# Optimization experiments

Measured on AMD Instinct MI355X. Metric: run time of the kernel, lower is better.

The kernel has to match this reference:

```python
import jax, jax.numpy as jnp
import numpy as np

HEAD_SIZE = 64


def setup_inputs() -> dict:
    key = jax.random.key(0)
    ks = jax.random.split(key, 4)
    B, S, H, D = 8, 4096, 768, HEAD_SIZE
    scale = 1.0 / np.sqrt(H)
    return {
        "x": jax.random.normal(ks[0], (B, S, H), dtype=jnp.float32),
        "Wq": jax.random.normal(ks[1], (H, D), dtype=jnp.float32) * scale,
        "bq": jnp.zeros((D,), dtype=jnp.float32),
        "Wk": jax.random.normal(ks[2], (H, D), dtype=jnp.float32) * scale,
        "bk": jnp.zeros((D,), dtype=jnp.float32),
        "Wv": jax.random.normal(ks[3], (H, D), dtype=jnp.float32) * scale,
        "bv": jnp.zeros((D,), dtype=jnp.float32),
    }


def reference(x, Wq, bq, Wk, bk, Wv, bv):
    # x: [B, S, H]
    B, S, H = x.shape
    D = Wq.shape[1]
    q = x @ Wq + bq  # [B, S, D]
    k = x @ Wk + bk
    v = x @ Wv + bv
    # naive full score matrix [B, S, S]
    scores = jnp.einsum("bsd,btd->bst", q, k)
    causal = jnp.tril(jnp.ones((S, S), dtype=bool))  # lower-triangular mask
    scores = jnp.where(causal[None, :, :], scores, -jnp.inf)
    attn = jax.nn.softmax(scores / jnp.sqrt(jnp.float32(D)), axis=-1)
    # dropout is identity in eval/deterministic reference
    out = jnp.einsum("bst,btd->bsd", attn, v)  # [B, S, D]
    return out
```

## Files before the change

kernel.cpp:

```cpp
#include <hip/hip_runtime.h>

typedef unsigned short u16;
typedef __bf16 bf16_t;
typedef bf16_t bf16x8 __attribute__((ext_vector_type(8)));
typedef float f32x4 __attribute__((ext_vector_type(4)));
typedef u16 u16x8 __attribute__((ext_vector_type(8)));

#define B_ 8
#define S_ 4096
#define H_ 768
#define M_ (B_ * S_)

__device__ __forceinline__ u16 f2b(float f) {
  unsigned u = __float_as_uint(f);
  u += 0x7fffu + ((u >> 16) & 1u);
  return (u16)(u >> 16);
}

__device__ __forceinline__ void gl_lds16(const void* g, void* l) {
  __builtin_amdgcn_global_load_lds(
      (const __attribute__((address_space(1))) void*)g,
      (__attribute__((address_space(3))) void*)l, 16, 0, 0);
}

__global__ __launch_bounds__(256) void wconv_k(const float* __restrict__ Wq,
                                               const float* __restrict__ Wk,
                                               const float* __restrict__ Wv,
                                               u16* __restrict__ WbT) {
  __shared__ float wt[64 * 68];
  const int tid = threadIdx.x;
  int mat = blockIdx.x / 12;
  int k0 = (blockIdx.x % 12) * 64;
  const float* W = (mat == 0) ? Wq : ((mat == 1) ? Wk : Wv);
  int r = tid >> 2, c0 = (tid & 3) * 16;
  const float* src = W + (size_t)(k0 + r) * 64 + c0;
#pragma unroll
  for (int j = 0; j < 16; j += 4)
    *(float4*)&wt[r * 68 + c0 + j] = *(const float4*)(src + j);
  __syncthreads();
  int d = tid >> 2;
  u16* dst = WbT + (size_t)(mat * 64 + d) * 768 + k0 + c0;
  u16x8 o0, o1;
#pragma unroll
  for (int j = 0; j < 8; ++j) o0[j] = f2b(wt[(c0 + j) * 68 + d]);
#pragma unroll
  for (int j = 0; j < 8; ++j) o1[j] = f2b(wt[(c0 + 8 + j) * 68 + d]);
  *(u16x8*)dst = o0;
  *(u16x8*)(dst + 8) = o1;
}

__global__ __launch_bounds__(256) void qkv_k(const float* __restrict__ x,
                                             const u16* __restrict__ WbT,
                                             const float* __restrict__ bq,
                                             const float* __restrict__ bk,
                                             const float* __restrict__ bv,
                                             u16* __restrict__ qb,
                                             u16* __restrict__ kb,
                                             u16* __restrict__ vbT) {
  __shared__ __align__(16) u16 smem[2 * 2560 + 2 * 7680];
  const int tid = threadIdx.x;
  const int w = tid >> 6, ln = tid & 15, qd = (tid >> 4) & 3;
  const int row0 = blockIdx.x * 64;

  const f32x4 z4 = {0.f, 0.f, 0.f, 0.f};
  f32x4 acc[4][3];
#pragma unroll
  for (int rt = 0; rt < 4; ++rt)
#pragma unroll
    for (int ct = 0; ct < 3; ++ct) acc[rt][ct] = z4;

  const int xr = tid >> 2, xc = (tid & 3) * 8;
  float4 xf0, xf1;
  u16x8 wf[3];

  auto load_t = [&](int kt) {
    const float* sx = x + (size_t)(row0 + xr) * 768 + kt * 32 + xc;
    xf0 = *(const float4*)sx;
    xf1 = *(const float4*)(sx + 4);
#pragma unroll
    for (int i = 0; i < 3; ++i) {
      int c = i * 256 + tid;
      int r = c >> 2, off = (c & 3) * 8;
      wf[i] = *(const u16x8*)(WbT + (size_t)r * 768 + kt * 32 + off);
    }
  };

  load_t(0);
  for (int kt = 0; kt < 24; ++kt) {
    u16* xs = smem + (kt & 1) * 2560;
    u16* wsb = smem + 5120 + (kt & 1) * 7680;
    {
      u16x8 v;
      v[0] = f2b(xf0.x); v[1] = f2b(xf0.y); v[2] = f2b(xf0.z); v[3] = f2b(xf0.w);
      v[4] = f2b(xf1.x); v[5] = f2b(xf1.y); v[6] = f2b(xf1.z); v[7] = f2b(xf1.w);
      *(u16x8*)&xs[xr * 40 + xc] = v;
#pragma unroll
      for (int i = 0; i < 3; ++i) {
        int c = i * 256 + tid;
        int r = c >> 2, off = (c & 3) * 8;
        *(u16x8*)&wsb[r * 40 + off] = wf[i];
      }
    }
    if (kt < 23) load_t(kt + 1);
    __syncthreads();
    bf16x8 af[4], bfr[3];
#pragma unroll
    for (int rt = 0; rt < 4; ++rt)
      af[rt] = *(const bf16x8*)&xs[(rt * 16 + ln) * 40 + qd * 8];
#pragma unroll
    for (int ct = 0; ct < 3; ++ct)
      bfr[ct] = *(const bf16x8*)&wsb[(w * 48 + ct * 16 + ln) * 40 + qd * 8];
#pragma unroll
    for (int rt = 0; rt < 4; ++rt)
#pragma unroll
      for (int ct = 0; ct < 3; ++ct)
        acc[rt][ct] = __builtin_amdgcn_mfma_f32_16x16x32_bf16(
            af[rt], bfr[ct], acc[rt][ct], 0, 0, 0);
    __syncthreads();
  }

  u16* vt = smem;
#pragma unroll
  for (int ct = 0; ct < 3; ++ct) {
    int col = w * 48 + ct * 16 + ln;
    int mat = col >> 6, d = col & 63;
    if (mat < 2) {
      const float* bp = (mat == 0) ? bq : bk;
      u16* op = (mat == 0) ? qb : kb;
      float bias = bp[d];
      float scale = (mat == 0) ? 0.18033688011112042f : 1.0f;
#pragma unroll
      for (int rt = 0; rt < 4; ++rt)
#pragma unroll
        for (int r = 0; r < 4; ++r)
          op[(size_t)(row0 + rt * 16 + qd * 4 + r) * 64 + d] =
              f2b((acc[rt][ct][r] + bias) * scale);
    } else {
      float bias = bv[d];
#pragma unroll
      for (int rt = 0; rt < 4; ++rt)
#pragma unroll
        for (int r = 0; r < 4; ++r)
          vt[d * 72 + rt * 16 + qd * 4 + r] = f2b(acc[rt][ct][r] + bias);
    }
  }
  __syncthreads();
  {
    int d = tid >> 2, so = (tid & 3) * 16;
    int b = row0 >> 12, s0 = row0 & 4095;
    u16* dst = vbT + ((size_t)b * 64 + d) * 4096 + s0 + so;
    *(u16x8*)dst = *(const u16x8*)&vt[d * 72 + so];
    *(u16x8*)(dst + 8) = *(const u16x8*)&vt[d * 72 + so + 8];
  }
}

__global__ __launch_bounds__(256) void attn_k(const u16* __restrict__ qb,
                                              const u16* __restrict__ kb,
                                              const u16* __restrict__ vbT,
                                              float* __restrict__ po0,
                                              float* __restrict__ po1,
                                              float* __restrict__ pl0,
                                              float* __restrict__ pl1) {
  __shared__ __align__(16) u16 ks[2][4096];
  __shared__ __align__(16) u16 vs[2][4096];
  __shared__ __align__(16) u16 ps[4 * 32 * 72];
  const int tid = threadIdx.x;
  const int w = tid >> 6, ln = tid & 15, qd = (tid >> 4) & 3;
  const int id = blockIdx.x;
  const int b = id & 7;
  const int j = id >> 3;
  const int qi = 31 - (j >> 1);
  const int chunk = j & 1;
  const int tstart = chunk ? (qi + 1) : 0;
  const int tcount = qi + 1;
  const int q0 = qi * 128;
  const int q0w = q0 + w * 32;
  const int base = b * S_;
  const u16* kg = kb + (size_t)base * 64;
  const u16* vg = vbT + (size_t)b * 64 * 4096;

  bf16x8 qf[2][2];
#pragma unroll
  for (int rt = 0; rt < 2; ++rt) {
    const u16* qrow = qb + (size_t)(base + q0w + rt * 16 + ln) * 64;
    qf[rt][0] = *(const bf16x8*)(qrow + qd * 8);
    qf[rt][1] = *(const bf16x8*)(qrow + 32 + qd * 8);
  }
  const f32x4 z4 = {0.f, 0.f, 0.f, 0.f};
  f32x4 o[2][4];
#pragma unroll
  for (int rt = 0; rt < 2; ++rt)
#pragma unroll
    for (int nt = 0; nt < 4; ++nt) o[rt][nt] = z4;
  float lp[2][4] = {{0.f, 0.f, 0.f, 0.f}, {0.f, 0.f, 0.f, 0.f}};
  u16* psw = ps + w * (32 * 72);
  const int lr = (tid & 63) >> 3, csl = tid & 7;

  auto prefetch = [&](int bufi, int tile) {
    const u16* kt_ = kg + (size_t)tile * 4096;
    const u16* vt_ = vg + tile * 64;
#pragma unroll
    for (int i = 0; i < 2; ++i) {
      int r0 = w * 16 + i * 8;
      int r = r0 + lr;
      int c = csl ^ (r & 7);
      gl_lds16(kt_ + r * 64 + c * 8, &ks[bufi][r0 * 64]);
      gl_lds16(vt_ + (size_t)r * 4096 + c * 8, &vs[bufi][r0 * 64]);
    }
  };

  prefetch(0, tstart);
  int buf = 0;
  for (int it = 0; it < tcount; ++it) {
    __syncthreads();
    if (it + 1 < tcount) prefetch(buf ^ 1, tstart + it + 1);
    const int t0a = (tstart + it) * 64;

    if (t0a <= q0w + 31) {
      f32x4 s0[4] = {z4, z4, z4, z4};
      f32x4 s1[4] = {z4, z4, z4, z4};
#pragma unroll
      for (int kc = 0; kc < 2; ++kc) {
        int cs = (kc * 4 + qd) ^ (ln & 7);
#pragma unroll
        for (int nt = 0; nt < 4; ++nt) {
          bf16x8 bfr = *(const bf16x8*)&ks[buf][(nt * 16 + ln) * 64 + cs * 8];
          s0[nt] = __builtin_amdgcn_mfma_f32_16x16x32_bf16(qf[0][kc], bfr, s0[nt], 0, 0, 0);
          s1[nt] = __builtin_amdgcn_mfma_f32_16x16x32_bf16(qf[1][kc], bfr, s1[nt], 0, 0, 0);
        }
      }
      if (t0a + 63 > q0w) {
#pragma unroll
        for (int nt = 0; nt < 4; ++nt) {
          int tg = t0a + nt * 16 + ln;
#pragma unroll
          for (int r = 0; r < 4; ++r) {
            if (tg > q0w + qd * 4 + r) s0[nt][r] = -INFINITY;
            if (tg > q0w + 16 + qd * 4 + r) s1[nt][r] = -INFINITY;
          }
        }
      }
#pragma unroll
      for (int nt = 0; nt < 4; ++nt)
#pragma unroll
        for (int r = 0; r < 4; ++r) {
          float p0 = __builtin_amdgcn_exp2f(s0[nt][r]);
          float p1 = __builtin_amdgcn_exp2f(s1[nt][r]);
          lp[0][r] += p0;
          lp[1][r] += p1;
          psw[(qd * 4 + r) * 72 + nt * 16 + ln] = f2b(p0);
          psw[(16 + qd * 4 + r) * 72 + nt * 16 + ln] = f2b(p1);
        }
#pragma unroll
      for (int kc = 0; kc < 2; ++kc) {
        bf16x8 a0 = *(const bf16x8*)&psw[ln * 72 + kc * 32 + qd * 8];
        bf16x8 a1 = *(const bf16x8*)&psw[(16 + ln) * 72 + kc * 32 + qd * 8];
        int cs = (kc * 4 + qd) ^ (ln & 7);
#pragma unroll
        for (int nt = 0; nt < 4; ++nt) {
          bf16x8 vfr = *(const bf16x8*)&vs[buf][(nt * 16 + ln) * 64 + cs * 8];
          o[0][nt] = __builtin_amdgcn_mfma_f32_16x16x32_bf16(a0, vfr, o[0][nt], 0, 0, 0);
          o[1][nt] = __builtin_amdgcn_mfma_f32_16x16x32_bf16(a1, vfr, o[1][nt], 0, 0, 0);
        }
      }
    }
    buf ^= 1;
  }

#pragma unroll
  for (int rt = 0; rt < 2; ++rt)
#pragma unroll
    for (int r = 0; r < 4; ++r) {
      float v = lp[rt][r];
      v += __shfl_xor(v, 1); v += __shfl_xor(v, 2);
      v += __shfl_xor(v, 4); v += __shfl_xor(v, 8);
      lp[rt][r] = v;
    }
  float* op = (tstart == 0) ? po0 : po1;
  float* lpt = (tstart == 0) ? pl0 : pl1;
#pragma unroll
  for (int rt = 0; rt < 2; ++rt)
#pragma unroll
    for (int r = 0; r < 4; ++r) {
      int row = base + q0w + rt * 16 + qd * 4 + r;
#pragma unroll
      for (int nt = 0; nt < 4; ++nt)
        op[(size_t)row * 64 + nt * 16 + ln] = o[rt][nt][r];
      if (ln == 0) lpt[row] = lp[rt][r];
    }
}

__global__ __launch_bounds__(256) void comb_k(const float* __restrict__ po0,
                                              const float* __restrict__ po1,
                                              const float* __restrict__ pl0,
                                              const float* __restrict__ pl1,
                                              float* __restrict__ out) {
  int idx = blockIdx.x * 256 + threadIdx.x;
  int r = idx >> 4, d0 = (idx & 15) * 4;
  float4 a = *(const float4*)(po0 + (size_t)r * 64 + d0);
  float4 c = *(const float4*)(po1 + (size_t)r * 64 + d0);
  float l = pl0[r] + pl1[r];
  float inv = 1.0f / l;
  a.x = (a.x + c.x) * inv;
  a.y = (a.y + c.y) * inv;
  a.z = (a.z + c.z) * inv;
  a.w = (a.w + c.w) * inv;
  *(float4*)(out + (size_t)r * 64 + d0) = a;
}

extern "C" void kernel_launch(void* const* d_in, const int* in_sizes, int n_in,
                              void* d_out, int out_size, void* d_ws, size_t ws_size,
                              hipStream_t stream) {
  const float* x  = (const float*)d_in[0];
  const float* Wq = (const float*)d_in[1];
  const float* bq = (const float*)d_in[2];
  const float* Wk = (const float*)d_in[3];
  const float* bk = (const float*)d_in[4];
  const float* Wv = (const float*)d_in[5];
  const float* bv = (const float*)d_in[6];
  float* out = (float*)d_out;

  char* wsp = (char*)d_ws;
  u16* WbT = (u16*)wsp;
  u16* qb  = (u16*)(wsp + 294912);
  u16* kb  = (u16*)(wsp + 4489216);
  u16* vbT = (u16*)(wsp + 8683520);
  float* po0 = (float*)(wsp + 12877824);
  float* po1 = (float*)(wsp + 21266432);
  float* pl0 = (float*)(wsp + 29655040);
  float* pl1 = (float*)(wsp + 29786112);

  hipLaunchKernelGGL(wconv_k, dim3(36), dim3(256), 0, stream, Wq, Wk, Wv, WbT);
  hipLaunchKernelGGL(qkv_k, dim3(512), dim3(256), 0, stream,
                     x, WbT, bq, bk, bv, qb, kb, vbT);
  hipLaunchKernelGGL(attn_k, dim3(512), dim3(256), 0, stream,
                     qb, kb, vbT, po0, po1, pl0, pl1);
  hipLaunchKernelGGL(comb_k, dim3(2048), dim3(256), 0, stream,
                     po0, po1, pl0, pl1, out);
}
```

Measured before the change: 234.1 us.

## Split attention KV range into variable chunks, triple-buffer tiles, transpose score MFMA

Replaces the fixed two-way split of each query block's key range with a variable number of chunks (1-4, scaled by causal length), launching 640 workgroups to balance work and fill the GPU better. The combine kernel sums the matching number of partial outputs and denominators. The K/V staging moves from double to triple buffering, with an explicit vmcnt wait instead of a full syncthreads. The QK MFMA operands are swapped so each lane holds a row's scores, which allows vectorized, XOR-swizzled P writes to LDS and fewer shuffles. The cost is more partial-output memory traffic and extra LDS use.

```diff
diff --git a/kernel.cpp b/kernel.cpp
--- a/kernel.cpp
+++ b/kernel.cpp
@@ -5,6 +5,7 @@
 typedef bf16_t bf16x8 __attribute__((ext_vector_type(8)));
 typedef float f32x4 __attribute__((ext_vector_type(4)));
 typedef u16 u16x8 __attribute__((ext_vector_type(8)));
+typedef u16 u16x4 __attribute__((ext_vector_type(4)));
 
 #define B_ 8
 #define S_ 4096
@@ -157,43 +158,46 @@
 __global__ __launch_bounds__(256) void attn_k(const u16* __restrict__ qb,
                                               const u16* __restrict__ kb,
                                               const u16* __restrict__ vbT,
-                                              float* __restrict__ po0,
-                                              float* __restrict__ po1,
-                                              float* __restrict__ pl0,
-                                              float* __restrict__ pl1) {
-  __shared__ __align__(16) u16 ks[2][4096];
-  __shared__ __align__(16) u16 vs[2][4096];
-  __shared__ __align__(16) u16 ps[4 * 32 * 72];
+                                              float* __restrict__ po,
+                                              float* __restrict__ pl) {
+  __shared__ __align__(16) u16 ks[3][4096];
+  __shared__ __align__(16) u16 vs[3][4096];
+  __shared__ __align__(16) u16 ps[4 * 32 * 64];
   const int tid = threadIdx.x;
-  const int w = tid >> 6, ln = tid & 15, qd = (tid >> 4) & 3;
+  const int wv = tid >> 6, ln = tid & 15, qd = (tid >> 4) & 3;
   const int id = blockIdx.x;
   const int b = id & 7;
   const int j = id >> 3;
-  const int qi = 31 - (j >> 1);
-  const int chunk = j & 1;
-  const int tstart = chunk ? (qi + 1) : 0;
-  const int tcount = qi + 1;
+  int qi = 31, acc = 0;
+  while (acc + ((qi >> 3) + 1) <= j) {
+    acc += (qi >> 3) + 1;
+    --qi;
+  }
+  const int c = j - acc;
+  const int ntiles = 2 * qi + 2;
+  const int nc = (qi >> 3) + 1;
+  const int bas = ntiles / nc, rem = ntiles % nc;
+  const int tstart = c * bas + (c < rem ? c : rem);
+  const int tcount = bas + (c < rem ? 1 : 0);
   const int q0 = qi * 128;
-  const int q0w = q0 + w * 32;
+  const int q0w = q0 + wv * 32;
   const int base = b * S_;
   const u16* kg = kb + (size_t)base * 64;
   const u16* vg = vbT + (size_t)b * 64 * 4096;
 
   bf16x8 qf[2][2];
 #pragma unroll
-  for (int rt = 0; rt < 2; ++rt) {
-    const u16* qrow = qb + (size_t)(base + q0w + rt * 16 + ln) * 64;
-    qf[rt][0] = *(const bf16x8*)(qrow + qd * 8);
-    qf[rt][1] = *(const bf16x8*)(qrow + 32 + qd * 8);
+  for (int qt = 0; qt < 2; ++qt) {
+    const u16* qrow = qb + (size_t)(base + q0w + qt * 16 + ln) * 64;
+    qf[qt][0] = *(const bf16x8*)(qrow + qd * 8);
+    qf[qt][1] = *(const bf16x8*)(qrow + 32 + qd * 8);
   }
   const f32x4 z4 = {0.f, 0.f, 0.f, 0.f};
-  f32x4 o[2][4];
-#pragma unroll
-  for (int rt = 0; rt < 2; ++rt)
-#pragma unroll
-    for (int nt = 0; nt < 4; ++nt) o[rt][nt] = z4;
-  float lp[2][4] = {{0.f, 0.f, 0.f, 0.f}, {0.f, 0.f, 0.f, 0.f}};
-  u16* psw = ps + w * (32 * 72);
+  f32x4 o0[4] = {z4, z4, z4, z4};
+  f32x4 o1[4] = {z4, z4, z4, z4};
+  float lq0 = 0.f, lq1 = 0.f;
+  u16* psw = ps + wv * 2048;
+  const int sw = (ln & 7) << 3;
   const int lr = (tid & 63) >> 3, csl = tid & 7;
 
   auto prefetch = [&](int bufi, int tile) {
@@ -201,19 +205,23 @@
     const u16* vt_ = vg + tile * 64;
 #pragma unroll
     for (int i = 0; i < 2; ++i) {
-      int r0 = w * 16 + i * 8;
+      int r0 = wv * 16 + i * 8;
       int r = r0 + lr;
-      int c = csl ^ (r & 7);
-      gl_lds16(kt_ + r * 64 + c * 8, &ks[bufi][r0 * 64]);
-      gl_lds16(vt_ + (size_t)r * 4096 + c * 8, &vs[bufi][r0 * 64]);
+      int cc = csl ^ (r & 7);
+      gl_lds16(kt_ + r * 64 + cc * 8, &ks[bufi][r0 * 64]);
+      gl_lds16(vt_ + (size_t)r * 4096 + cc * 8, &vs[bufi][r0 * 64]);
     }
   };
 
   prefetch(0, tstart);
-  int buf = 0;
+  prefetch(1, tstart + (tcount > 1 ? 1 : 0));
+  int cur = 0, pfb = 2;
   for (int it = 0; it < tcount; ++it) {
-    __syncthreads();
-    if (it + 1 < tcount) prefetch(buf ^ 1, tstart + it + 1);
+    asm volatile("s_waitcnt vmcnt(4)" ::: "memory");
+    __builtin_amdgcn_s_barrier();
+    int nx = it + 2;
+    nx = nx < tcount ? nx : tcount - 1;
+    prefetch(pfb, tstart + nx);
     const int t0a = (tstart + it) * 64;
 
     if (t0a <= q0w + 31) {
@@ -224,87 +232,106 @@
         int cs = (kc * 4 + qd) ^ (ln & 7);
 #pragma unroll
         for (int nt = 0; nt < 4; ++nt) {
-          bf16x8 bfr = *(const bf16x8*)&ks[buf][(nt * 16 + ln) * 64 + cs * 8];
-          s0[nt] = __builtin_amdgcn_mfma_f32_16x16x32_bf16(qf[0][kc], bfr, s0[nt], 0, 0, 0);
-          s1[nt] = __builtin_amdgcn_mfma_f32_16x16x32_bf16(qf[1][kc], bfr, s1[nt], 0, 0, 0);
+          bf16x8 kf = *(const bf16x8*)&ks[cur][(nt * 16 + ln) * 64 + cs * 8];
+          s0[nt] = __builtin_amdgcn_mfma_f32_16x16x32_bf16(kf, qf[0][kc], s0[nt], 0, 0, 0);
+          s1[nt] = __builtin_amdgcn_mfma_f32_16x16x32_bf16(kf, qf[1][kc], s1[nt], 0, 0, 0);
         }
       }
       if (t0a + 63 > q0w) {
 #pragma unroll
         for (int nt = 0; nt < 4; ++nt) {
-          int tg = t0a + nt * 16 + ln;
+          int tg = t0a + nt * 16 + qd * 4;
 #pragma unroll
           for (int r = 0; r < 4; ++r) {
-            if (tg > q0w + qd * 4 + r) s0[nt][r] = -INFINITY;
-            if (tg > q0w + 16 + qd * 4 + r) s1[nt][r] = -INFINITY;
+            if (tg + r > q0w + ln) s0[nt][r] = -INFINITY;
+            if (tg + r > q0w + 16 + ln) s1[nt][r] = -INFINITY;
           }
         }
       }
 #pragma unroll
-      for (int nt = 0; nt < 4; ++nt)
+      for (int nt = 0; nt < 4; ++nt) {
+        u16x4 w0, w1;
 #pragma unroll
         for (int r = 0; r < 4; ++r) {
           float p0 = __builtin_amdgcn_exp2f(s0[nt][r]);
           float p1 = __builtin_amdgcn_exp2f(s1[nt][r]);
-          lp[0][r] += p0;
-          lp[1][r] += p1;
-          psw[(qd * 4 + r) * 72 + nt * 16 + ln] = f2b(p0);
-          psw[(16 + qd * 4 + r) * 72 + nt * 16 + ln] = f2b(p1);
+          lq0 += p0;
+          lq1 += p1;
+          w0[r] = f2b(p0);
+          w1[r] = f2b(p1);
         }
+        int off = (nt * 16 + qd * 4) ^ sw;
+        *(u16x4*)&psw[ln * 64 + off] = w0;
+        *(u16x4*)&psw[(16 + ln) * 64 + off] = w1;
+      }
 #pragma unroll
       for (int kc = 0; kc < 2; ++kc) {
-        bf16x8 a0 = *(const bf16x8*)&psw[ln * 72 + kc * 32 + qd * 8];
-        bf16x8 a1 = *(const bf16x8*)&psw[(16 + ln) * 72 + kc * 32 + qd * 8];
+        int poff = (kc * 32 + qd * 8) ^ sw;
+        bf16x8 a0 = *(const bf16x8*)&psw[ln * 64 + poff];
+        bf16x8 a1 = *(const bf16x8*)&psw[(16 + ln) * 64 + poff];
         int cs = (kc * 4 + qd) ^ (ln & 7);
 #pragma unroll
         for (int nt = 0; nt < 4; ++nt) {
-          bf16x8 vfr = *(const bf16x8*)&vs[buf][(nt * 16 + ln) * 64 + cs * 8];
-          o[0][nt] = __builtin_amdgcn_mfma_f32_16x16x32_bf16(a0, vfr, o[0][nt], 0, 0, 0);
-          o[1][nt] = __builtin_amdgcn_mfma_f32_16x16x32_bf16(a1, vfr, o[1][nt], 0, 0, 0);
+          bf16x8 vf = *(const bf16x8*)&vs[cur][(nt * 16 + ln) * 64 + cs * 8];
+          o0[nt] = __builtin_amdgcn_mfma_f32_16x16x32_bf16(a0, vf, o0[nt], 0, 0, 0);
+          o1[nt] = __builtin_amdgcn_mfma_f32_16x16x32_bf16(a1, vf, o1[nt], 0, 0, 0);
         }
       }
     }
-    buf ^= 1;
-  }
-
-#pragma unroll
-  for (int rt = 0; rt < 2; ++rt)
-#pragma unroll
-    for (int r = 0; r < 4; ++r) {
-      float v = lp[rt][r];
-      v += __shfl_xor(v, 1); v += __shfl_xor(v, 2);
-      v += __shfl_xor(v, 4); v += __shfl_xor(v, 8);
-      lp[rt][r] = v;
-    }
-  float* op = (tstart == 0) ? po0 : po1;
-  float* lpt = (tstart == 0) ? pl0 : pl1;
-#pragma unroll
-  for (int rt = 0; rt < 2; ++rt)
-#pragma unroll
-    for (int r = 0; r < 4; ++r) {
-      int row = base + q0w + rt * 16 + qd * 4 + r;
-#pragma unroll
-      for (int nt = 0; nt < 4; ++nt)
-        op[(size_t)row * 64 + nt * 16 + ln] = o[rt][nt][r];
-      if (ln == 0) lpt[row] = lp[rt][r];
-    }
-}
-
-__global__ __launch_bounds__(256) void comb_k(const float* __restrict__ po0,
-                                              const float* __restrict__ po1,
-                                              const float* __restrict__ pl0,
-                                              const float* __restrict__ pl1,
+    cur = (cur == 2) ? 0 : cur + 1;
+    pfb = (pfb == 2) ? 0 : pfb + 1;
+  }
+
+  lq0 += __shfl_xor(lq0, 16);
+  lq0 += __shfl_xor(lq0, 32);
+  lq1 += __shfl_xor(lq1, 16);
+  lq1 += __shfl_xor(lq1, 32);
+
+  float* op = po + (size_t)c * 2097152;
+  float* lpt = pl + (size_t)c * 32768;
+#pragma unroll
+  for (int r = 0; r < 4; ++r) {
+    int row0 = base + q0w + qd * 4 + r;
+    int row1 = row0 + 16;
+#pragma unroll
+    for (int nt = 0; nt < 4; ++nt) {
+      op[(size_t)row0 * 64 + nt * 16 + ln] = o0[nt][r];
+      op[(size_t)row1 * 64 + nt * 16 + ln] = o1[nt][r];
+    }
+  }
+  if (qd == 0) {
+    lpt[base + q0w + ln] = lq0;
+    lpt[base + q0w + 16 + ln] = lq1;
+  }
+}
+
+__global__ __launch_bounds__(256) void comb_k(const float* __restrict__ po,
+                                              const float* __restrict__ pl,
                                               float* __restrict__ out) {
   int idx = blockIdx.x * 256 + threadIdx.x;
   int r = idx >> 4, d0 = (idx & 15) * 4;
-  float4 a = *(const float4*)(po0 + (size_t)r * 64 + d0);
-  float4 c = *(const float4*)(po1 + (size_t)r * 64 + d0);
-  float l = pl0[r] + pl1[r];
+  int qi = (r & 4095) >> 7;
+  int nc = (qi >> 3) + 1;
+  const float* p = po + (size_t)r * 64 + d0;
+  float4 a = *(const float4*)p;
+  float l = pl[r];
+  if (nc > 1) {
+    float4 t = *(const float4*)(p + 2097152);
+    a.x += t.x; a.y += t.y; a.z += t.z; a.w += t.w;
+    l += pl[r + 32768];
+  }
+  if (nc > 2) {
+    float4 t = *(const float4*)(p + 4194304);
+    a.x += t.x; a.y += t.y; a.z += t.z; a.w += t.w;
+    l += pl[r + 65536];
+  }
+  if (nc > 3) {
+    float4 t = *(const float4*)(p + 6291456);
+    a.x += t.x; a.y += t.y; a.z += t.z; a.w += t.w;
+    l += pl[r + 98304];
+  }
   float inv = 1.0f / l;
-  a.x = (a.x + c.x) * inv;
-  a.y = (a.y + c.y) * inv;
-  a.z = (a.z + c.z) * inv;
-  a.w = (a.w + c.w) * inv;
+  a.x *= inv; a.y *= inv; a.z *= inv; a.w *= inv;
   *(float4*)(out + (size_t)r * 64 + d0) = a;
 }
 
@@ -325,16 +352,14 @@
   u16* qb  = (u16*)(wsp + 294912);
   u16* kb  = (u16*)(wsp + 4489216);
   u16* vbT = (u16*)(wsp + 8683520);
-  float* po0 = (float*)(wsp + 12877824);
-  float* po1 = (float*)(wsp + 21266432);
-  float* pl0 = (float*)(wsp + 29655040);
-  float* pl1 = (float*)(wsp + 29786112);
+  float* po = (float*)(wsp + 12877824);
+  float* pl = (float*)(wsp + 46432256);
 
   hipLaunchKernelGGL(wconv_k, dim3(36), dim3(256), 0, stream, Wq, Wk, Wv, WbT);
   hipLaunchKernelGGL(qkv_k, dim3(512), dim3(256), 0, stream,
                      x, WbT, bq, bk, bv, qb, kb, vbT);
-  hipLaunchKernelGGL(attn_k, dim3(512), dim3(256), 0, stream,
-                     qb, kb, vbT, po0, po1, pl0, pl1);
+  hipLaunchKernelGGL(attn_k, dim3(640), dim3(256), 0, stream,
+                     qb, kb, vbT, po, pl);
   hipLaunchKernelGGL(comb_k, dim3(2048), dim3(256), 0, stream,
-                     po0, po1, pl0, pl1, out);
-}
+                     po, pl, out);
+}
```

Measured after the change: 224.6 us. 4.1% less time.
